# Optimization experiments

Measured on AMD Instinct MI355X. Metric: run time of the kernel, lower is better.

Reference implementation:

```python
import jax, jax.numpy as jnp
import numpy as np

N = 100_000      # nodes
F_IN = 512       # input feature dim
HID = 8          # hidden per head (layer 1)
HEADS = 8        # heads layer 1
CLS = 7          # num classes (layer 2 out, 1 head)
E = 1_600_000    # random edges (self-loops added in reference)
NEG_SLOPE = 0.2  # PyG GATConv default leaky_relu slope


def setup_inputs() -> dict:
    key = jax.random.key(0)
    ks = jax.random.split(key, 10)
    s1 = 1.0 / np.sqrt(F_IN)
    s2 = 1.0 / np.sqrt(HID * HEADS)
    return {
        "x": jax.random.normal(ks[0], (N, F_IN), jnp.float32),
        "edge_index": jax.random.randint(ks[1], (2, E), 0, N, dtype=jnp.int32),
        "W1": jax.random.normal(ks[2], (F_IN, HEADS * HID), jnp.float32) * s1,
        "a_src1": jax.random.normal(ks[3], (HEADS, HID), jnp.float32) * s1,
        "a_dst1": jax.random.normal(ks[4], (HEADS, HID), jnp.float32) * s1,
        "b1": jnp.zeros((HEADS * HID,), jnp.float32),
        "W2": jax.random.normal(ks[5], (HEADS * HID, CLS), jnp.float32) * s2,
        "a_src2": jax.random.normal(ks[6], (1, CLS), jnp.float32) * s2,
        "a_dst2": jax.random.normal(ks[7], (1, CLS), jnp.float32) * s2,
        "b2": jnp.zeros((CLS,), jnp.float32),
    }


def gat_layer(x, edge_index, W, a_src, a_dst, bias, concat):
    """PyG GATConv (eval mode): linear -> per-edge LeakyReLU score -> edge-softmax over
    incoming edges per dst node -> weighted scatter-sum of src messages."""
    n = x.shape[0]
    H, C = a_src.shape
    h = (x @ W).reshape(n, H, C)                      # [N, H, C]
    src, dst = edge_index[0], edge_index[1]
    alpha_src = (h * a_src).sum(-1)                   # [N, H]
    alpha_dst = (h * a_dst).sum(-1)                   # [N, H]
    e = jax.nn.leaky_relu(alpha_src[src] + alpha_dst[dst], NEG_SLOPE)  # [E, H]
    # numerically stable segment softmax over edges grouped by dst
    m = jax.ops.segment_max(e, dst, num_segments=n)   # [N, H]
    p = jnp.exp(e - m[dst])                           # [E, H]
    denom = jax.ops.segment_sum(p, dst, num_segments=n)
    alpha = p / denom[dst]                            # [E, H]
    out = jax.ops.segment_sum(alpha[:, :, None] * h[src], dst, num_segments=n)  # [N, H, C]
    out = out.reshape(n, H * C) if concat else out.mean(axis=1)
    return out + bias


def reference(x, edge_index, W1, a_src1, a_dst1, b1, W2, a_src2, a_dst2, b2):
    # add self-loops (GATConv default add_self_loops=True)
    loops = jnp.arange(N, dtype=edge_index.dtype)
    ei = jnp.concatenate([edge_index, jnp.stack([loops, loops])], axis=1)
    h = jax.nn.elu(gat_layer(x, ei, W1, a_src1, a_dst1, b1, concat=True))
    out = gat_layer(h, ei, W2, a_src2, a_dst2, b2, concat=False)
    return jax.nn.log_softmax(out, axis=1)
```

## Files before the change

kernel.cpp:

```cpp
#include <hip/hip_runtime.h>
#include <hip/hip_bf16.h>

#define NEG_SLOPE 0.2f
#define SBK 256

typedef __attribute__((ext_vector_type(8))) short bfrag;
typedef __attribute__((ext_vector_type(4))) float f32x4;
typedef unsigned short ushort_t;

__device__ __forceinline__ float lrelu(float x) {
    return x >= 0.0f ? x : NEG_SLOPE * x;
}
__device__ __forceinline__ unsigned short f2bf(float f) {
    unsigned int u = __float_as_uint(f);
    u += 0x7fffu + ((u >> 16) & 1u);
    return (unsigned short)(u >> 16);
}
__device__ __forceinline__ float bf2f(unsigned short h) {
    return __uint_as_float(((unsigned int)h) << 16);
}
__device__ __forceinline__ float u2lo(unsigned int u) {
    return __uint_as_float(u << 16);
}
__device__ __forceinline__ float u2hi(unsigned int u) {
    return __uint_as_float(u & 0xffff0000u);
}

__global__ __launch_bounds__(256) void hist_prep_kernel(
    const int* __restrict__ edst, int* __restrict__ cnt2d, int E, int NB,
    const float* __restrict__ W1, ushort_t* __restrict__ Whi,
    ushort_t* __restrict__ Wlo) {
    if (blockIdx.x < 128) {
        int t = blockIdx.x * 256 + threadIdx.x;
        int k = t >> 6, c = t & 63;
        float w = W1[t];
        unsigned short hi = f2bf(w);
        float rem = w - bf2f(hi);
        int dst = (k >> 7) * 8192 + c * 128 + (k & 127);
        Whi[dst] = hi;
        Wlo[dst] = f2bf(rem);
        return;
    }
    __shared__ int hist[512];
    int tid = threadIdx.x;
    for (int i = tid; i < 512; i += 256) hist[i] = 0;
    __syncthreads();
    int s = blockIdx.x - 128;
    int CH = (E + SBK - 1) / SBK;
    int st = s * CH, en = min(st + CH, E);
    for (int i = st + tid; i < en; i += 256)
        atomicAdd(&hist[edst[i] >> 8], 1);
    __syncthreads();
    for (int b = tid; b < NB; b += 256)
        cnt2d[b * SBK + s] = hist[b];
}

__global__ __launch_bounds__(256) void scan_cols_kernel(
    int* __restrict__ cnt2d, int* __restrict__ bcnt, int NB) {
    int b = blockIdx.x;
    int t = threadIdx.x;
    __shared__ int sc[256];
    int v = cnt2d[b * SBK + t];
    sc[t] = v;
    __syncthreads();
    for (int off = 1; off < 256; off <<= 1) {
        int tv = (t >= off) ? sc[t - off] : 0;
        __syncthreads();
        sc[t] += tv;
        __syncthreads();
    }
    cnt2d[b * SBK + t] = sc[t] - v;
    if (t == 255) bcnt[b] = sc[255];
}

__global__ __launch_bounds__(512) void bscan_kernel(
    const int* __restrict__ bcnt, int* __restrict__ boff,
    int* __restrict__ csr_off, int NB, int N, int E) {
    __shared__ int s[512];
    int t = threadIdx.x;
    int v = (t < NB) ? bcnt[t] : 0;
    s[t] = v;
    __syncthreads();
    for (int off = 1; off < 512; off <<= 1) {
        int tv = (t >= off) ? s[t - off] : 0;
        __syncthreads();
        s[t] += tv;
        __syncthreads();
    }
    if (t < NB) boff[t] = s[t] - v;
    if (t == 0) {
        boff[NB] = E;
        csr_off[N] = E;
    }
}

__global__ __launch_bounds__(1024) void scatter_kernel(
    const int* __restrict__ esrc, const int* __restrict__ edst,
    const int* __restrict__ boff, const int* __restrict__ cnt2d,
    int* __restrict__ ebuf, int E, int NB) {
    __shared__ int base[512];
    __shared__ int rank[512];
    int tid = threadIdx.x;
    int s = blockIdx.x;
    for (int b = tid; b < NB; b += 1024) {
        base[b] = boff[b] + cnt2d[b * SBK + s];
        rank[b] = 0;
    }
    __syncthreads();
    int CH = (E + SBK - 1) / SBK;
    int st = s * CH, en = min(st + CH, E);
    for (int i = st + tid; i < en; i += 1024) {
        int d = edst[i];
        int b = d >> 8;
        int r = atomicAdd(&rank[b], 1);
        ebuf[base[b] + r] = (esrc[i] << 8) | (d & 255);
    }
}

__global__ __launch_bounds__(1024, 4) void gemm_kernel(
    const float* __restrict__ x, const ushort_t* __restrict__ Whi,
    const ushort_t* __restrict__ Wlo, ushort_t* __restrict__ h1b, int n,
    const float* __restrict__ a_src1, const float* __restrict__ a_dst1,
    float* __restrict__ as1, float* __restrict__ ad1) {
    __shared__ __align__(16) ushort_t Wh[32768];
    __shared__ __align__(16) ushort_t Wl[32768];
    const int tid = threadIdx.x;

    #pragma unroll
    for (int i = 0; i < 4; i++) {
        int lin = (tid + i * 1024) * 8;
        int row = (lin >> 7) & 63;
        int swz = lin ^ ((row & 7) << 3);
        *(bfrag*)&Wh[swz] = *(const bfrag*)&Whi[lin];
        *(bfrag*)&Wl[swz] = *(const bfrag*)&Wlo[lin];
    }
    __syncthreads();

    const int lane = tid & 63;
    const int wave = tid >> 6;
    const int l15 = lane & 15;
    const int lq = lane >> 4;
    const int r7s = (l15 & 7) << 3;

    const int ntiles = (n + 15) >> 4;
    const int tstride = 256 * 16;

    for (int tile = blockIdx.x * 16 + wave; tile < ntiles; tile += tstride) {
        const int wb = tile * 16;
        f32x4 acc[4];
        #pragma unroll
        for (int t = 0; t < 4; t++) acc[t] = (f32x4){0.f, 0.f, 0.f, 0.f};

        const int arow = min(wb + l15, n - 1);
        const float* xr = x + (size_t)arow * 512;

        #pragma unroll 1
        for (int p = 0; p < 4; p++) {
            #pragma unroll
            for (int step = 0; step < 4; step++) {
                int kloc = step * 32 + lq * 8;
                int kb = p * 128 + kloc;
                float4 v0 = *(const float4*)&xr[kb];
                float4 v1 = *(const float4*)&xr[kb + 4];
                float xf[8] = {v0.x, v0.y, v0.z, v0.w, v1.x, v1.y, v1.z, v1.w};
                bfrag ah, al;
                #pragma unroll
                for (int j = 0; j < 8; j++) {
                    unsigned short hi = f2bf(xf[j]);
                    float rem = xf[j] - bf2f(hi);
                    ah[j] = (short)hi;
                    al[j] = (short)f2bf(rem);
                }
                #pragma unroll
                for (int t = 0; t < 4; t++) {
                    int nrow = t * 16 + l15;
                    int bidx = ((p * 64 + nrow) * 128 + kloc) ^ r7s;
                    bfrag bh = *(const bfrag*)&Wh[bidx];
                    bfrag bl = *(const bfrag*)&Wl[bidx];
                    acc[t] = __builtin_amdgcn_mfma_f32_16x16x32_bf16(al, bh, acc[t], 0, 0, 0);
                    acc[t] = __builtin_amdgcn_mfma_f32_16x16x32_bf16(ah, bl, acc[t], 0, 0, 0);
                    acc[t] = __builtin_amdgcn_mfma_f32_16x16x32_bf16(ah, bh, acc[t], 0, 0, 0);
                }
            }
        }
        #pragma unroll
        for (int t = 0; t < 4; t++) {
            #pragma unroll
            for (int reg = 0; reg < 4; reg++) {
                int grow = wb + lq * 4 + reg;
                if (grow < n) h1b[(size_t)grow * 64 + t * 16 + l15] = f2bf(acc[t][reg]);
            }
        }
        const int j7 = l15 & 7;
        const int wrow = wb + lq * 4 + (j7 & 3);
        #pragma unroll
        for (int t = 0; t < 4; t++) {
            int cidx = t * 16 + l15;
            float cs = a_src1[cidx];
            float cd = a_dst1[cidx];
            float ps0 = acc[t][0] * cs, ps1 = acc[t][1] * cs;
            float ps2 = acc[t][2] * cs, ps3 = acc[t][3] * cs;
            float pd0 = acc[t][0] * cd, pd1 = acc[t][1] * cd;
            float pd2 = acc[t][2] * cd, pd3 = acc[t][3] * cd;
            #pragma unroll
            for (int off = 1; off < 8; off <<= 1) {
                ps0 += __shfl_xor(ps0, off);
                ps1 += __shfl_xor(ps1, off);
                ps2 += __shfl_xor(ps2, off);
                ps3 += __shfl_xor(ps3, off);
                pd0 += __shfl_xor(pd0, off);
                pd1 += __shfl_xor(pd1, off);
                pd2 += __shfl_xor(pd2, off);
                pd3 += __shfl_xor(pd3, off);
            }
            int h = (t << 1) | (l15 >> 3);
            if (wrow < n) {
                if (j7 < 4) {
                    float sv = j7 == 0 ? ps0 : j7 == 1 ? ps1 : j7 == 2 ? ps2 : ps3;
                    as1[wrow * 8 + h] = sv;
                } else {
                    float dv = j7 == 4 ? pd0 : j7 == 5 ? pd1 : j7 == 6 ? pd2 : pd3;
                    ad1[wrow * 8 + h] = dv;
                }
            }
        }
    }
}

__global__ __launch_bounds__(256) void finalize_kernel(
    const int* __restrict__ boff, const int* __restrict__ ebuf,
    int* __restrict__ csr_off, int* __restrict__ col, int N, int NB) {
    int tid = threadIdx.x;
    int b = blockIdx.x;
    __shared__ int cnt[256];
    __shared__ int cur[256];
    __shared__ int sc[256];
    cnt[tid] = 0;
    __syncthreads();
    int st = boff[b], en = boff[b + 1];
    for (int i = st + tid; i < en; i += 256)
        atomicAdd(&cnt[ebuf[i] & 255], 1);
    __syncthreads();
    int v = cnt[tid];
    sc[tid] = v;
    __syncthreads();
    for (int off = 1; off < 256; off <<= 1) {
        int tv = (tid >= off) ? sc[tid - off] : 0;
        __syncthreads();
        sc[tid] += tv;
        __syncthreads();
    }
    int dbase = b << 8;
    int nd = min(256, N - dbase);
    int o = st + sc[tid] - v;
    if (tid < nd) {
        csr_off[dbase + tid] = o;
        cur[tid] = o;
    }
    __syncthreads();
    for (int i = st + tid; i < en; i += 256) {
        int p = ebuf[i];
        int r = atomicAdd(&cur[p & 255], 1);
        col[r] = ((unsigned int)p) >> 8;
    }
}

__global__ __launch_bounds__(256) void agg1_kernel(
    const int* __restrict__ csr_off, const int* __restrict__ col,
    const ushort_t* __restrict__ h1b, const float* __restrict__ as1,
    const float* __restrict__ ad1,
    const float* __restrict__ b1, const float* __restrict__ W2,
    const float* __restrict__ a_src2, const float* __restrict__ a_dst2,
    float* __restrict__ g2, float* __restrict__ ad2, int n) {
    int d = blockIdx.x * 8 + (threadIdx.x >> 5);
    if (d >= n) return;
    int c = threadIdx.x & 31;
    int hd = c >> 2;
    const ushort_t* myrow = h1b + (size_t)d * 64;
    float adh = ad1[d * 8 + hd];
    float asd = as1[d * 8 + hd];
    float p0 = __expf(lrelu(asd + adh));
    unsigned int u = *(const unsigned int*)(myrow + c * 2);
    float denom = p0;
    float acc0 = p0 * u2lo(u);
    float acc1 = p0 * u2hi(u);
    int st = csr_off[d], en = csr_off[d + 1];
    int e = st;
    for (; e + 4 <= en; e += 4) {
        int s0 = col[e], s1 = col[e + 1], s2 = col[e + 2], s3 = col[e + 3];
        const ushort_t* r0 = h1b + (size_t)s0 * 64;
        const ushort_t* r1 = h1b + (size_t)s1 * 64;
        const ushort_t* r2 = h1b + (size_t)s2 * 64;
        const ushort_t* r3 = h1b + (size_t)s3 * 64;
        float a0 = as1[s0 * 8 + hd];
        float a1 = as1[s1 * 8 + hd];
        float a2 = as1[s2 * 8 + hd];
        float a3 = as1[s3 * 8 + hd];
        unsigned int u0 = *(const unsigned int*)(r0 + c * 2);
        unsigned int u1 = *(const unsigned int*)(r1 + c * 2);
        unsigned int u2 = *(const unsigned int*)(r2 + c * 2);
        unsigned int u3 = *(const unsigned int*)(r3 + c * 2);
        float q0 = __expf(lrelu(a0 + adh));
        float q1 = __expf(lrelu(a1 + adh));
        float q2 = __expf(lrelu(a2 + adh));
        float q3 = __expf(lrelu(a3 + adh));
        denom += (q0 + q1) + (q2 + q3);
        acc0 = fmaf(q0, u2lo(u0), acc0);
        acc1 = fmaf(q0, u2hi(u0), acc1);
        acc0 = fmaf(q1, u2lo(u1), acc0);
        acc1 = fmaf(q1, u2hi(u1), acc1);
        acc0 = fmaf(q2, u2lo(u2), acc0);
        acc1 = fmaf(q2, u2hi(u2), acc1);
        acc0 = fmaf(q3, u2lo(u3), acc0);
        acc1 = fmaf(q3, u2hi(u3), acc1);
    }
    for (; e < en; ++e) {
        int s0 = col[e];
        const ushort_t* r0 = h1b + (size_t)s0 * 64;
        float a0 = as1[s0 * 8 + hd];
        unsigned int u0 = *(const unsigned int*)(r0 + c * 2);
        float q0 = __expf(lrelu(a0 + adh));
        denom += q0;
        acc0 = fmaf(q0, u2lo(u0), acc0);
        acc1 = fmaf(q0, u2hi(u0), acc1);
    }
    float v0 = acc0 / denom + b1[2 * c];
    float v1 = acc1 / denom + b1[2 * c + 1];
    float h0 = v0 > 0.f ? v0 : (__expf(v0) - 1.f);
    float h1v = v1 > 0.f ? v1 : (__expf(v1) - 1.f);
    float g[7];
    #pragma unroll
    for (int j = 0; j < 7; j++) {
        float t = fmaf(h0, W2[(2 * c) * 7 + j], h1v * W2[(2 * c + 1) * 7 + j]);
        #pragma unroll
        for (int off = 1; off < 32; off <<= 1) t += __shfl_xor(t, off);
        g[j] = t;
    }
    float sa = 0.f, da = 0.f;
    #pragma unroll
    for (int j = 0; j < 7; j++) {
        sa = fmaf(g[j], a_src2[j], sa);
        da = fmaf(g[j], a_dst2[j], da);
    }
    if (c < 7) g2[(size_t)d * 8 + c] = g[c];
    if (c == 7) g2[(size_t)d * 8 + 7] = sa;
    if (c == 8) ad2[d] = da;
}

__global__ __launch_bounds__(256) void agg2_kernel(
    const int* __restrict__ csr_off, const int* __restrict__ col,
    const float* __restrict__ ad2, const float* __restrict__ g2,
    const float* __restrict__ b2, float* __restrict__ out, int n) {
    int d = blockIdx.x * 4 + (threadIdx.x >> 6);
    if (d >= n) return;
    int lane = threadIdx.x & 63;
    int j = lane >> 3, cc = lane & 7;
    int bl = lane | 7;
    float adv = ad2[d];
    float vd = g2[(size_t)d * 8 + cc];
    float as2d = __shfl(vd, bl);
    float pd = (j == 0) ? __expf(lrelu(as2d + adv)) : 0.f;
    float denom = pd;
    float acc = pd * vd;
    int st = csr_off[d], en = csr_off[d + 1];
    for (int base = st; base < en; base += 8) {
        int eidx = base + j;
        bool valid = eidx < en;
        int s = valid ? col[eidx] : d;
        float val = g2[(size_t)s * 8 + cc];
        float as2s = __shfl(val, bl);
        float p = valid ? __expf(lrelu(as2s + adv)) : 0.f;
        denom += p;
        acc = fmaf(p, val, acc);
    }
    #pragma unroll
    for (int off = 8; off < 64; off <<= 1) {
        acc += __shfl_xor(acc, off);
        denom += __shfl_xor(denom, off);
    }
    float o = acc / denom + ((cc < 7) ? b2[cc] : 0.f);
    float m = (cc < 7) ? o : -1e30f;
    #pragma unroll
    for (int off = 1; off < 8; off <<= 1) m = fmaxf(m, __shfl_xor(m, off));
    float se = (cc < 7) ? __expf(o - m) : 0.f;
    #pragma unroll
    for (int off = 1; off < 8; off <<= 1) se += __shfl_xor(se, off);
    float lse = m + __logf(se);
    if (j == 0 && cc < 7) out[(size_t)d * 7 + cc] = o - lse;
}

extern "C" void kernel_launch(void* const* d_in, const int* in_sizes, int n_in,
                              void* d_out, int out_size, void* d_ws, size_t ws_size,
                              hipStream_t stream) {
    const float* x      = (const float*)d_in[0];
    const int*   ei     = (const int*)d_in[1];
    const float* W1     = (const float*)d_in[2];
    const float* a_src1 = (const float*)d_in[3];
    const float* a_dst1 = (const float*)d_in[4];
    const float* b1     = (const float*)d_in[5];
    const float* W2     = (const float*)d_in[6];
    const float* a_src2 = (const float*)d_in[7];
    const float* a_dst2 = (const float*)d_in[8];
    const float* b2     = (const float*)d_in[9];

    int N = in_sizes[0] / 512;
    int E = in_sizes[1] / 2;
    const int* esrc = ei;
    const int* edst = ei + E;
    int NB = (N + 255) >> 8;

    char* ws = (char*)d_ws;
    size_t off = 0;
    auto alloc = [&](size_t bytes) -> void* {
        void* p = ws + off;
        off += (bytes + 255) & ~(size_t)255;
        return p;
    };
    ushort_t* h1b  = (ushort_t*)alloc((size_t)N * 64 * 2);
    float* as1     = (float*)alloc((size_t)N * 8 * 4);
    float* ad1     = (float*)alloc((size_t)N * 8 * 4);
    float* g2      = (float*)alloc((size_t)N * 8 * 4);
    float* ad2     = (float*)alloc((size_t)N * 4);
    int*   csr_off = (int*)alloc((size_t)(N + 1) * 4);
    int*   col     = (int*)alloc((size_t)E * 4);
    int*   ebuf    = (int*)alloc((size_t)E * 4);
    ushort_t* Whi  = (ushort_t*)alloc(512 * 64 * 2);
    ushort_t* Wlo  = (ushort_t*)alloc(512 * 64 * 2);
    int*   cnt2d   = (int*)alloc((size_t)NB * SBK * 4);
    int*   bcnt    = (int*)alloc((size_t)NB * 4);
    int*   boff    = (int*)alloc((size_t)(NB + 1) * 4);

    hist_prep_kernel<<<128 + SBK, 256, 0, stream>>>(edst, cnt2d, E, NB, W1, Whi, Wlo);
    scan_cols_kernel<<<NB, 256, 0, stream>>>(cnt2d, bcnt, NB);
    bscan_kernel<<<1, 512, 0, stream>>>(bcnt, boff, csr_off, NB, N, E);
    scatter_kernel<<<SBK, 1024, 0, stream>>>(esrc, edst, boff, cnt2d, ebuf, E, NB);
    gemm_kernel<<<256, 1024, 0, stream>>>(x, Whi, Wlo, h1b, N,
                                          a_src1, a_dst1, as1, ad1);
    finalize_kernel<<<NB, 256, 0, stream>>>(boff, ebuf, csr_off, col, N, NB);
    agg1_kernel<<<(N + 7) / 8, 256, 0, stream>>>(csr_off, col, h1b, as1, ad1, b1,
                                                 W2, a_src2, a_dst2, g2, ad2, N);
    agg2_kernel<<<(N + 3) / 4, 256, 0, stream>>>(csr_off, col, ad2, g2, b2,
                                                 (float*)d_out, N);
}
```

Measured before the change: 463.7 us.

## Process two row tiles per wave in GEMM and widen agg1 per-lane features

The GEMM wave now computes two 16-row tiles at once, so each LDS load of the W hi/lo fragments feeds six MFMAs instead of three, halving LDS traffic per output. Separately, agg1 now gives each destination node 16 lanes, each loading 4 bf16 features with a 64-bit load, instead of 32 lanes with 2 features each. Fewer lanes per node means more nodes per block and fewer shuffle steps in the W2 reduction. The cost is higher register pressure in the GEMM and less memory-level parallelism per node in agg1.

```diff
diff --git a/kernel.cpp b/kernel.cpp
--- a/kernel.cpp
+++ b/kernel.cpp
@@ -143,16 +143,22 @@
     const int r7s = (l15 & 7) << 3;
 
     const int ntiles = (n + 15) >> 4;
-    const int tstride = 256 * 16;
-
-    for (int tile = blockIdx.x * 16 + wave; tile < ntiles; tile += tstride) {
-        const int wb = tile * 16;
-        f32x4 acc[4];
+    const int npairs = (ntiles + 1) >> 1;
+    const int pstride = 256 * 16;
+
+    for (int pair = blockIdx.x * 16 + wave; pair < npairs; pair += pstride) {
+        const int wb = pair * 32;
+        f32x4 acc0[4], acc1[4];
         #pragma unroll
-        for (int t = 0; t < 4; t++) acc[t] = (f32x4){0.f, 0.f, 0.f, 0.f};
-
-        const int arow = min(wb + l15, n - 1);
-        const float* xr = x + (size_t)arow * 512;
+        for (int t = 0; t < 4; t++) {
+            acc0[t] = (f32x4){0.f, 0.f, 0.f, 0.f};
+            acc1[t] = (f32x4){0.f, 0.f, 0.f, 0.f};
+        }
+
+        const int ar0 = min(wb + l15, n - 1);
+        const int ar1 = min(wb + 16 + l15, n - 1);
+        const float* xr0 = x + (size_t)ar0 * 512;
+        const float* xr1 = x + (size_t)ar1 * 512;
 
         #pragma unroll 1
         for (int p = 0; p < 4; p++) {
@@ -160,16 +166,21 @@
             for (int step = 0; step < 4; step++) {
                 int kloc = step * 32 + lq * 8;
                 int kb = p * 128 + kloc;
-                float4 v0 = *(const float4*)&xr[kb];
-                float4 v1 = *(const float4*)&xr[kb + 4];
-                float xf[8] = {v0.x, v0.y, v0.z, v0.w, v1.x, v1.y, v1.z, v1.w};
-                bfrag ah, al;
+                float4 a0 = *(const float4*)&xr0[kb];
+                float4 a1 = *(const float4*)&xr0[kb + 4];
+                float4 b0 = *(const float4*)&xr1[kb];
+                float4 b1v = *(const float4*)&xr1[kb + 4];
+                float xf0[8] = {a0.x, a0.y, a0.z, a0.w, a1.x, a1.y, a1.z, a1.w};
+                float xf1[8] = {b0.x, b0.y, b0.z, b0.w, b1v.x, b1v.y, b1v.z, b1v.w};
+                bfrag ah0, al0, ah1, al1;
                 #pragma unroll
                 for (int j = 0; j < 8; j++) {
-                    unsigned short hi = f2bf(xf[j]);
-                    float rem = xf[j] - bf2f(hi);
-                    ah[j] = (short)hi;
-                    al[j] = (short)f2bf(rem);
+                    unsigned short h0 = f2bf(xf0[j]);
+                    al0[j] = (short)f2bf(xf0[j] - bf2f(h0));
+                    ah0[j] = (short)h0;
+                    unsigned short h1 = f2bf(xf1[j]);
+                    al1[j] = (short)f2bf(xf1[j] - bf2f(h1));
+                    ah1[j] = (short)h1;
                 }
                 #pragma unroll
                 for (int t = 0; t < 4; t++) {
@@ -177,50 +188,58 @@
                     int bidx = ((p * 64 + nrow) * 128 + kloc) ^ r7s;
                     bfrag bh = *(const bfrag*)&Wh[bidx];
                     bfrag bl = *(const bfrag*)&Wl[bidx];
-                    acc[t] = __builtin_amdgcn_mfma_f32_16x16x32_bf16(al, bh, acc[t], 0, 0, 0);
-                    acc[t] = __builtin_amdgcn_mfma_f32_16x16x32_bf16(ah, bl, acc[t], 0, 0, 0);
-                    acc[t] = __builtin_amdgcn_mfma_f32_16x16x32_bf16(ah, bh, acc[t], 0, 0, 0);
+                    acc0[t] = __builtin_amdgcn_mfma_f32_16x16x32_bf16(al0, bh, acc0[t], 0, 0, 0);
+                    acc0[t] = __builtin_amdgcn_mfma_f32_16x16x32_bf16(ah0, bl, acc0[t], 0, 0, 0);
+                    acc0[t] = __builtin_amdgcn_mfma_f32_16x16x32_bf16(ah0, bh, acc0[t], 0, 0, 0);
+                    acc1[t] = __builtin_amdgcn_mfma_f32_16x16x32_bf16(al1, bh, acc1[t], 0, 0, 0);
+                    acc1[t] = __builtin_amdgcn_mfma_f32_16x16x32_bf16(ah1, bl, acc1[t], 0, 0, 0);
+                    acc1[t] = __builtin_amdgcn_mfma_f32_16x16x32_bf16(ah1, bh, acc1[t], 0, 0, 0);
                 }
             }
         }
         #pragma unroll
-        for (int t = 0; t < 4; t++) {
+        for (int half = 0; half < 2; half++) {
+            const f32x4* acc = half ? acc1 : acc0;
+            const int tb = wb + half * 16;
             #pragma unroll
-            for (int reg = 0; reg < 4; reg++) {
-                int grow = wb + lq * 4 + reg;
-                if (grow < n) h1b[(size_t)grow * 64 + t * 16 + l15] = f2bf(acc[t][reg]);
+            for (int t = 0; t < 4; t++) {
+                #pragma unroll
+                for (int reg = 0; reg < 4; reg++) {
+                    int grow = tb + lq * 4 + reg;
+                    if (grow < n) h1b[(size_t)grow * 64 + t * 16 + l15] = f2bf(acc[t][reg]);
+                }
             }
-        }
-        const int j7 = l15 & 7;
-        const int wrow = wb + lq * 4 + (j7 & 3);
-        #pragma unroll
-        for (int t = 0; t < 4; t++) {
-            int cidx = t * 16 + l15;
-            float cs = a_src1[cidx];
-            float cd = a_dst1[cidx];
-            float ps0 = acc[t][0] * cs, ps1 = acc[t][1] * cs;
-            float ps2 = acc[t][2] * cs, ps3 = acc[t][3] * cs;
-            float pd0 = acc[t][0] * cd, pd1 = acc[t][1] * cd;
-            float pd2 = acc[t][2] * cd, pd3 = acc[t][3] * cd;
+            const int j7 = l15 & 7;
+            const int wrow = tb + lq * 4 + (j7 & 3);
             #pragma unroll
-            for (int off = 1; off < 8; off <<= 1) {
-                ps0 += __shfl_xor(ps0, off);
-                ps1 += __shfl_xor(ps1, off);
-                ps2 += __shfl_xor(ps2, off);
-                ps3 += __shfl_xor(ps3, off);
-                pd0 += __shfl_xor(pd0, off);
-                pd1 += __shfl_xor(pd1, off);
-                pd2 += __shfl_xor(pd2, off);
-                pd3 += __shfl_xor(pd3, off);
-            }
-            int h = (t << 1) | (l15 >> 3);
-            if (wrow < n) {
-                if (j7 < 4) {
-                    float sv = j7 == 0 ? ps0 : j7 == 1 ? ps1 : j7 == 2 ? ps2 : ps3;
-                    as1[wrow * 8 + h] = sv;
-                } else {
-                    float dv = j7 == 4 ? pd0 : j7 == 5 ? pd1 : j7 == 6 ? pd2 : pd3;
-                    ad1[wrow * 8 + h] = dv;
+            for (int t = 0; t < 4; t++) {
+                int cidx = t * 16 + l15;
+                float cs = a_src1[cidx];
+                float cd = a_dst1[cidx];
+                float ps0 = acc[t][0] * cs, ps1 = acc[t][1] * cs;
+                float ps2 = acc[t][2] * cs, ps3 = acc[t][3] * cs;
+                float pd0 = acc[t][0] * cd, pd1 = acc[t][1] * cd;
+                float pd2 = acc[t][2] * cd, pd3 = acc[t][3] * cd;
+                #pragma unroll
+                for (int off = 1; off < 8; off <<= 1) {
+                    ps0 += __shfl_xor(ps0, off);
+                    ps1 += __shfl_xor(ps1, off);
+                    ps2 += __shfl_xor(ps2, off);
+                    ps3 += __shfl_xor(ps3, off);
+                    pd0 += __shfl_xor(pd0, off);
+                    pd1 += __shfl_xor(pd1, off);
+                    pd2 += __shfl_xor(pd2, off);
+                    pd3 += __shfl_xor(pd3, off);
+                }
+                int h = (t << 1) | (l15 >> 3);
+                if (wrow < n) {
+                    if (j7 < 4) {
+                        float sv = j7 == 0 ? ps0 : j7 == 1 ? ps1 : j7 == 2 ? ps2 : ps3;
+                        as1[wrow * 8 + h] = sv;
+                    } else {
+                        float dv = j7 == 4 ? pd0 : j7 == 5 ? pd1 : j7 == 6 ? pd2 : pd3;
+                        ad1[wrow * 8 + h] = dv;
+                    }
                 }
             }
         }
@@ -272,18 +291,20 @@
     const float* __restrict__ b1, const float* __restrict__ W2,
     const float* __restrict__ a_src2, const float* __restrict__ a_dst2,
     float* __restrict__ g2, float* __restrict__ ad2, int n) {
-    int d = blockIdx.x * 8 + (threadIdx.x >> 5);
+    int d = blockIdx.x * 16 + (threadIdx.x >> 4);
     if (d >= n) return;
-    int c = threadIdx.x & 31;
-    int hd = c >> 2;
+    int c16 = threadIdx.x & 15;
+    int hd = c16 >> 1;
     const ushort_t* myrow = h1b + (size_t)d * 64;
     float adh = ad1[d * 8 + hd];
     float asd = as1[d * 8 + hd];
     float p0 = __expf(lrelu(asd + adh));
-    unsigned int u = *(const unsigned int*)(myrow + c * 2);
+    uint2 uu = *(const uint2*)(myrow + c16 * 4);
     float denom = p0;
-    float acc0 = p0 * u2lo(u);
-    float acc1 = p0 * u2hi(u);
+    float acc0 = p0 * u2lo(uu.x);
+    float acc1 = p0 * u2hi(uu.x);
+    float acc2 = p0 * u2lo(uu.y);
+    float acc3 = p0 * u2hi(uu.y);
     int st = csr_off[d], en = csr_off[d + 1];
     int e = st;
     for (; e + 4 <= en; e += 4) {
@@ -296,44 +317,62 @@
         float a1 = as1[s1 * 8 + hd];
         float a2 = as1[s2 * 8 + hd];
         float a3 = as1[s3 * 8 + hd];
-        unsigned int u0 = *(const unsigned int*)(r0 + c * 2);
-        unsigned int u1 = *(const unsigned int*)(r1 + c * 2);
-        unsigned int u2 = *(const unsigned int*)(r2 + c * 2);
-        unsigned int u3 = *(const unsigned int*)(r3 + c * 2);
+        uint2 u0 = *(const uint2*)(r0 + c16 * 4);
+        uint2 u1 = *(const uint2*)(r1 + c16 * 4);
+        uint2 u2 = *(const uint2*)(r2 + c16 * 4);
+        uint2 u3 = *(const uint2*)(r3 + c16 * 4);
         float q0 = __expf(lrelu(a0 + adh));
         float q1 = __expf(lrelu(a1 + adh));
         float q2 = __expf(lrelu(a2 + adh));
         float q3 = __expf(lrelu(a3 + adh));
         denom += (q0 + q1) + (q2 + q3);
-        acc0 = fmaf(q0, u2lo(u0), acc0);
-        acc1 = fmaf(q0, u2hi(u0), acc1);
-        acc0 = fmaf(q1, u2lo(u1), acc0);
-        acc1 = fmaf(q1, u2hi(u1), acc1);
-        acc0 = fmaf(q2, u2lo(u2), acc0);
-        acc1 = fmaf(q2, u2hi(u2), acc1);
-        acc0 = fmaf(q3, u2lo(u3), acc0);
-        acc1 = fmaf(q3, u2hi(u3), acc1);
+        acc0 = fmaf(q0, u2lo(u0.x), acc0);
+        acc1 = fmaf(q0, u2hi(u0.x), acc1);
+        acc2 = fmaf(q0, u2lo(u0.y), acc2);
+        acc3 = fmaf(q0, u2hi(u0.y), acc3);
+        acc0 = fmaf(q1, u2lo(u1.x), acc0);
+        acc1 = fmaf(q1, u2hi(u1.x), acc1);
+        acc2 = fmaf(q1, u2lo(u1.y), acc2);
+        acc3 = fmaf(q1, u2hi(u1.y), acc3);
+        acc0 = fmaf(q2, u2lo(u2.x), acc0);
+        acc1 = fmaf(q2, u2hi(u2.x), acc1);
+        acc2 = fmaf(q2, u2lo(u2.y), acc2);
+        acc3 = fmaf(q2, u2hi(u2.y), acc3);
+        acc0 = fmaf(q3, u2lo(u3.x), acc0);
+        acc1 = fmaf(q3, u2hi(u3.x), acc1);
+        acc2 = fmaf(q3, u2lo(u3.y), acc2);
+        acc3 = fmaf(q3, u2hi(u3.y), acc3);
     }
     for (; e < en; ++e) {
         int s0 = col[e];
         const ushort_t* r0 = h1b + (size_t)s0 * 64;
         float a0 = as1[s0 * 8 + hd];
-        unsigned int u0 = *(const unsigned int*)(r0 + c * 2);
+        uint2 u0 = *(const uint2*)(r0 + c16 * 4);
         float q0 = __expf(lrelu(a0 + adh));
         denom += q0;
-        acc0 = fmaf(q0, u2lo(u0), acc0);
-        acc1 = fmaf(q0, u2hi(u0), acc1);
-    }
-    float v0 = acc0 / denom + b1[2 * c];
-    float v1 = acc1 / denom + b1[2 * c + 1];
+        acc0 = fmaf(q0, u2lo(u0.x), acc0);
+        acc1 = fmaf(q0, u2hi(u0.x), acc1);
+        acc2 = fmaf(q0, u2lo(u0.y), acc2);
+        acc3 = fmaf(q0, u2hi(u0.y), acc3);
+    }
+    int f0 = c16 * 4;
+    float v0 = acc0 / denom + b1[f0];
+    float v1 = acc1 / denom + b1[f0 + 1];
+    float v2 = acc2 / denom + b1[f0 + 2];
+    float v3 = acc3 / denom + b1[f0 + 3];
     float h0 = v0 > 0.f ? v0 : (__expf(v0) - 1.f);
-    float h1v = v1 > 0.f ? v1 : (__expf(v1) - 1.f);
+    float h1 = v1 > 0.f ? v1 : (__expf(v1) - 1.f);
+    float h2 = v2 > 0.f ? v2 : (__expf(v2) - 1.f);
+    float h3 = v3 > 0.f ? v3 : (__expf(v3) - 1.f);
     float g[7];
     #pragma unroll
     for (int j = 0; j < 7; j++) {
-        float t = fmaf(h0, W2[(2 * c) * 7 + j], h1v * W2[(2 * c + 1) * 7 + j]);
+        float t = h0 * W2[f0 * 7 + j];
+        t = fmaf(h1, W2[(f0 + 1) * 7 + j], t);
+        t = fmaf(h2, W2[(f0 + 2) * 7 + j], t);
+        t = fmaf(h3, W2[(f0 + 3) * 7 + j], t);
         #pragma unroll
-        for (int off = 1; off < 32; off <<= 1) t += __shfl_xor(t, off);
+        for (int off = 1; off < 16; off <<= 1) t += __shfl_xor(t, off);
         g[j] = t;
     }
     float sa = 0.f, da = 0.f;
@@ -342,9 +381,9 @@
         sa = fmaf(g[j], a_src2[j], sa);
         da = fmaf(g[j], a_dst2[j], da);
     }
-    if (c < 7) g2[(size_t)d * 8 + c] = g[c];
-    if (c == 7) g2[(size_t)d * 8 + 7] = sa;
-    if (c == 8) ad2[d] = da;
+    if (c16 < 7) g2[(size_t)d * 8 + c16] = g[c16];
+    if (c16 == 7) g2[(size_t)d * 8 + 7] = sa;
+    if (c16 == 8) ad2[d] = da;
 }
 
 __global__ __launch_bounds__(256) void agg2_kernel(
@@ -437,8 +476,8 @@
     gemm_kernel<<<256, 1024, 0, stream>>>(x, Whi, Wlo, h1b, N,
                                           a_src1, a_dst1, as1, ad1);
     finalize_kernel<<<NB, 256, 0, stream>>>(boff, ebuf, csr_off, col, N, NB);
-    agg1_kernel<<<(N + 7) / 8, 256, 0, stream>>>(csr_off, col, h1b, as1, ad1, b1,
-                                                 W2, a_src2, a_dst2, g2, ad2, N);
+    agg1_kernel<<<(N + 15) / 16, 256, 0, stream>>>(csr_off, col, h1b, as1, ad1, b1,
+                                                   W2, a_src2, a_dst2, g2, ad2, N);
     agg2_kernel<<<(N + 3) / 4, 256, 0, stream>>>(csr_off, col, ad2, g2, b2,
                                                  (float*)d_out, N);
 }
```

Result: no change. 455.7 us (-1.7%).
